# Optimization experiments

Hardware: AMD Instinct MI355X
Metric: run time of the kernel (lower is better)

## Reference

```python
import jax, jax.numpy as jnp
import numpy as np

B, L, DIN, H, E, K = 64, 256, 768, 64, 8, 2
S = 16  # sqrt(L): token<->feature grid side
LOSS_COEF = 1e-2


def gelu(x):
    return jax.nn.gelu(x, approximate=False)  # torch nn.GELU (exact erf)


def cv_squared(v):
    v = v.astype(jnp.float32)
    return jnp.var(v, ddof=1) / (jnp.mean(v) ** 2 + 1e-10)


def setup_inputs() -> dict:
    key = jax.random.key(0)
    ks = jax.random.split(key, 16)
    rn = lambda k, shape, s=0.02: jax.random.normal(k, shape, jnp.float32) * s
    lap = jnp.array([[0., 1., 0.], [1., -4., 1.], [0., 1., 0.]], jnp.float32)
    return {
        "x": jax.random.normal(ks[0], (B, L, DIN), jnp.float32),
        "dte": jax.random.normal(ks[1], (B, L, DIN), jnp.float32),
        "w_gate": rn(ks[2], (L, E), 1.0),
        "W_exp": rn(ks[3], (E, DIN, H)), "b_exp": jnp.zeros((E, H), jnp.float32),
        "W_sh": rn(ks[4], (DIN, H)), "b_sh": jnp.zeros((H,), jnp.float32),
        "ln_g": jnp.ones((H,), jnp.float32), "ln_b": jnp.zeros((H,), jnp.float32),
        "W_px": rn(ks[5], (H, 2 * H)), "b_px": jnp.zeros((2 * H,), jnp.float32),
        "conv_sh": jnp.tile(lap[None, None], (H, 1, 1, 1)),  # depthwise Laplacian [H,1,3,3]
        "W_pxx": rn(ks[6], (H, H)), "b_pxx": jnp.zeros((H,), jnp.float32),
        "W_dte": rn(ks[7], (H, H)), "b_dte": jnp.zeros((H,), jnp.float32),
        "W_dteall": rn(ks[8], (H, H)), "b_dteall": jnp.zeros((H,), jnp.float32),
        "W_rgb": rn(ks[9], (DIN, H)), "b_rgb": jnp.zeros((H,), jnp.float32),
        "W_fx": rn(ks[10], (H, H)), "b_fx": jnp.zeros((H,), jnp.float32),
        "W_fmod": rn(ks[11], (H, H)), "b_fmod": jnp.zeros((H,), jnp.float32),
        "W_fxx": rn(ks[12], (H, H)), "b_fxx": jnp.zeros((H,), jnp.float32),
    }


def reference(x, dte, w_gate, W_exp, b_exp, W_sh, b_sh, ln_g, ln_b, W_px, b_px,
              conv_sh, W_pxx, b_pxx, W_dte, b_dte, W_dteall, b_dteall,
              W_rgb, b_rgb, W_fx, b_fx, W_fmod, b_fmod, W_fxx, b_fxx):
    # ---- top-k gating (clean logits; noisy_gating=False / eval) ----
    logits = dte.mean(-1) @ w_gate                     # [B,E]
    topv, topi = jax.lax.top_k(logits, K)
    topg = jax.nn.softmax(topv, axis=1)
    gates = jnp.zeros_like(logits).at[jnp.arange(B)[:, None], topi].set(topg)
    importance = gates.sum(0)
    load = (gates > 0).sum(0).astype(jnp.float32)
    loss = LOSS_COEF * (cv_squared(importance) + cv_squared(load))
    # ---- sparse dispatch / expert Linear / weighted combine (dense-equivalent) ----
    y = jnp.einsum('be,bld,edh->blh', gates, dte, W_exp) + (gates @ b_exp)[:, None, :]
    # ---- shared expert Linear + Shared block ----
    sh = dte @ W_sh + b_sh                             # [B,L,H]
    shortcut = sh
    t = (sh - sh.mean(-1, keepdims=True)) * jax.lax.rsqrt(sh.var(-1, keepdims=True) + 1e-6)
    t = t * ln_g + ln_b
    t = t @ W_px + b_px                                # [B,L,2H]
    t1, t2 = t[..., :H], t[..., H:]
    f = t1.transpose(0, 2, 1).reshape(B, H, S, S)      # token2feature
    f = jax.lax.conv_general_dilated(f, conv_sh, (1, 1), 'SAME', feature_group_count=H)
    t1 = f.reshape(B, H, L).transpose(0, 2, 1)         # feature2token
    sh = (gelu(t1) * t2) @ W_pxx + b_pxx + shortcut
    # ---- combine MoE and shared streams ----
    dte_tok = (y @ W_dte + b_dte) + (sh @ W_dteall + b_dteall)
    rgb_tok = x @ W_rgb + b_rgb
    # ---- Fusion (its self.norm was overwritten to GELU; token<->feature round-trip is identity) ----
    shortcut = rgb_tok
    a = gelu(rgb_tok) @ W_fx + b_fx
    m = gelu(dte_tok) @ W_fmod + b_fmod
    out = (gelu(m) * a) @ W_fxx + b_fxx + shortcut     # [B,L,H]
    return out, loss
```

## Files before the change

kernel.cpp:

```cpp
#include <hip/hip_runtime.h>
#include <hip/hip_bf16.h>
#include <math.h>

typedef unsigned short u16;
typedef unsigned int u32;
typedef __attribute__((ext_vector_type(8))) short bf16x8;
typedef __attribute__((ext_vector_type(4))) float f32x4;


__device__ __forceinline__ float bf2f(u16 u) {
    union { u32 i; float f; } x; x.i = ((u32)u) << 16; return x.f;
}
__device__ __forceinline__ u16 f2bf(float f) {
    union { __hip_bfloat16 h; u16 u; } x;
    x.h = __float2bfloat16(f);
    return x.u;
}
__device__ __forceinline__ u32 pack2(float a, float b) {
    union { __hip_bfloat162 h; u32 u; } x;
    x.h = __float22bfloat162_rn(make_float2(a, b));
    return x.u;
}
__device__ __forceinline__ float wsum(float v) {
    #pragma unroll
    for (int o = 1; o < 64; o <<= 1) v += __shfl_xor(v, o, 64);
    return v;
}
__device__ __forceinline__ float gelu_f(float x) {
    return 0.5f * x * (1.0f + erff(x * 0.70710678118654752440f));
}

__global__ __launch_bounds__(256) void k_gate_part(const float* __restrict__ dte,
                                                   const float* __restrict__ w_gate,
                                                   float* __restrict__ partial) {
    __shared__ float dmeanS[64];
    int p = blockIdx.x, tid = threadIdx.x, w = tid >> 6, lane = tid & 63;
    #pragma unroll
    for (int h = 0; h < 2; h++) {
        float4 v[8][3];
        #pragma unroll
        for (int i = 0; i < 8; i++) {
            const float* pr = dte + ((size_t)p * 64 + w * 16 + h * 8 + i) * 768;
            #pragma unroll
            for (int j = 0; j < 3; j++)
                v[i][j] = *(const float4*)(pr + (lane + j * 64) * 4);
        }
        #pragma unroll
        for (int i = 0; i < 8; i++) {
            float s = 0.f;
            #pragma unroll
            for (int j = 0; j < 3; j++)
                s += v[i][j].x + v[i][j].y + v[i][j].z + v[i][j].w;
            s = wsum(s);
            if (lane == 0) dmeanS[w * 16 + h * 8 + i] = s * (1.f / 768.f);
        }
    }
    __syncthreads();
    if (w == 0) {
        float dm = dmeanS[lane];
        int wl = (p & 3) * 64 + lane;
        #pragma unroll
        for (int e = 0; e < 8; e++) {
            float s = wsum(dm * w_gate[wl * 8 + e]);
            if (lane == 0) partial[p * 8 + e] = s;
        }
    }
}

__global__ __launch_bounds__(256) void k_gate_fin(const float* __restrict__ partial,
                                                  const float* __restrict__ b_exp,
                                                  int* __restrict__ topi,
                                                  float* __restrict__ topg,
                                                  float* __restrict__ bias_y,
                                                  float* __restrict__ loss_out) {
    __shared__ float gS[64 * 8];
    __shared__ int i0S[64], i1S[64];
    __shared__ float g0S[64], g1S[64];
    int tid = threadIdx.x;
    if (tid < 64) {
        float lg[8];
        #pragma unroll
        for (int e = 0; e < 8; e++)
            lg[e] = partial[(tid * 4 + 0) * 8 + e] + partial[(tid * 4 + 1) * 8 + e] +
                    partial[(tid * 4 + 2) * 8 + e] + partial[(tid * 4 + 3) * 8 + e];
        int i0 = 0; float v0 = lg[0];
        #pragma unroll
        for (int e = 1; e < 8; e++) if (lg[e] > v0) { v0 = lg[e]; i0 = e; }
        int i1 = -1; float v1 = -1e30f;
        #pragma unroll
        for (int e = 0; e < 8; e++) if (e != i0 && lg[e] > v1) { v1 = lg[e]; i1 = e; }
        if (i1 < 0) i1 = (i0 + 1) & 7;
        float e2 = expf(v1 - v0);
        float g0 = 1.f / (1.f + e2);
        float g1 = e2 / (1.f + e2);
        #pragma unroll
        for (int e = 0; e < 8; e++) gS[tid * 8 + e] = 0.f;
        gS[tid * 8 + i0] = g0;
        gS[tid * 8 + i1] = g1;
        i0S[tid] = i0; i1S[tid] = i1; g0S[tid] = g0; g1S[tid] = g1;
        topi[tid * 2] = i0; topi[tid * 2 + 1] = i1;
        topg[tid * 2] = g0; topg[tid * 2 + 1] = g1;
    }
    __syncthreads();
    for (int idx = tid; idx < 4096; idx += 256) {
        int b = idx >> 6, h = idx & 63;
        bias_y[idx] = g0S[b] * b_exp[i0S[b] * 64 + h] + g1S[b] * b_exp[i1S[b] * 64 + h];
    }
    if (tid < 64) {
        float g[8];
        #pragma unroll
        for (int e = 0; e < 8; e++) g[e] = gS[tid * 8 + e];
        float imp[8], ld[8];
        #pragma unroll
        for (int e = 0; e < 8; e++) {
            imp[e] = wsum(g[e]);
            ld[e]  = wsum(g[e] > 0.f ? 1.f : 0.f);
        }
        if (tid == 0) {
            float l = 0.f;
            {
                float s = 0.f;
                #pragma unroll
                for (int e = 0; e < 8; e++) s += imp[e];
                float mn = s / 8.f, v = 0.f;
                #pragma unroll
                for (int e = 0; e < 8; e++) { float d = imp[e] - mn; v += d * d; }
                l += (v / 7.f) / (mn * mn + 1e-10f);
            }
            {
                float s = 0.f;
                #pragma unroll
                for (int e = 0; e < 8; e++) s += ld[e];
                float mn = s / 8.f, v = 0.f;
                #pragma unroll
                for (int e = 0; e < 8; e++) { float d = ld[e] - mn; v += d * d; }
                l += (v / 7.f) / (mn * mn + 1e-10f);
            }
            loss_out[0] = 0.01f * l;
        }
    }
}

__global__ __launch_bounds__(256) void k_gemm3(const float* __restrict__ dte,
                                               const float* __restrict__ x,
                                               const float* __restrict__ W_sh,
                                               const float* __restrict__ b_sh,
                                               const float* __restrict__ W_exp,
                                               const int* __restrict__ topi,
                                               const float* __restrict__ topg,
                                               const float* __restrict__ bias_y,
                                               const float* __restrict__ W_rgb,
                                               const float* __restrict__ b_rgb,
                                               float* __restrict__ buf_sh,
                                               u16* __restrict__ buf_y,
                                               float* __restrict__ out_rgb) {
    __shared__ __align__(16) u16 As[64 * 72];
    __shared__ __align__(16) u16 Wt0[64 * 72];
    __shared__ __align__(16) u16 Wt1[64 * 72];
    int bid = blockIdx.x;
    bool fused = bid < 256;
    int row0 = fused ? bid * 64 : (bid - 256) * 64;
    int b = row0 >> 8;
    int tid = threadIdx.x, wv = tid >> 6, lane = tid & 63;
    int m = lane & 15, quad = lane >> 4;

    const float* A  = fused ? dte : x;
    const float* Wb = fused ? W_sh : W_rgb;
    const float* We0 = W_exp;
    const float* We1 = W_exp;
    float g0 = 0.f, g1 = 0.f;
    if (fused) {
        We0 = W_exp + (size_t)topi[2 * b] * 49152;
        We1 = W_exp + (size_t)topi[2 * b + 1] * 49152;
        g0 = topg[2 * b]; g1 = topg[2 * b + 1];
    }

    float4 pa[2][2];
    float4 pwv0[4];
    float4 pwv1[4];
    const int a_r  = tid >> 3;
    const int a_k8 = (tid & 7) * 8;
    const int wn4  = (tid & 15) * 4;
    const int wk4  = (tid >> 4) * 4;

    auto loadA = [&](int kc) {
        #pragma unroll
        for (int j = 0; j < 2; j++) {
            const float* src = A + (size_t)(row0 + a_r + j * 32) * 768 + kc * 64 + a_k8;
            pa[j][0] = *(const float4*)(src);
            pa[j][1] = *(const float4*)(src + 4);
        }
    };
    auto loadW = [&](int kc) {
        #pragma unroll
        for (int q = 0; q < 4; q++)
            pwv0[q] = *(const float4*)(Wb + (size_t)(kc * 64 + wk4 + q) * 64 + wn4);
        if (fused) {
            #pragma unroll
            for (int q = 0; q < 4; q++) {
                float4 a = *(const float4*)(We0 + (size_t)(kc * 64 + wk4 + q) * 64 + wn4);
                float4 c = *(const float4*)(We1 + (size_t)(kc * 64 + wk4 + q) * 64 + wn4);
                pwv1[q] = make_float4(g0 * a.x + g1 * c.x, g0 * a.y + g1 * c.y,
                                      g0 * a.z + g1 * c.z, g0 * a.w + g1 * c.w);
            }
        }
    };
    auto stageLDS = [&]() {
        #pragma unroll
        for (int j = 0; j < 2; j++) {
            uint4 d;
            d.x = pack2(pa[j][0].x, pa[j][0].y);
            d.y = pack2(pa[j][0].z, pa[j][0].w);
            d.z = pack2(pa[j][1].x, pa[j][1].y);
            d.w = pack2(pa[j][1].z, pa[j][1].w);
            *(uint4*)&As[(a_r + j * 32) * 72 + a_k8] = d;
        }
        *(uint2*)&Wt0[(wn4 + 0) * 72 + wk4] =
            make_uint2(pack2(pwv0[0].x, pwv0[1].x), pack2(pwv0[2].x, pwv0[3].x));
        *(uint2*)&Wt0[(wn4 + 1) * 72 + wk4] =
            make_uint2(pack2(pwv0[0].y, pwv0[1].y), pack2(pwv0[2].y, pwv0[3].y));
        *(uint2*)&Wt0[(wn4 + 2) * 72 + wk4] =
            make_uint2(pack2(pwv0[0].z, pwv0[1].z), pack2(pwv0[2].z, pwv0[3].z));
        *(uint2*)&Wt0[(wn4 + 3) * 72 + wk4] =
            make_uint2(pack2(pwv0[0].w, pwv0[1].w), pack2(pwv0[2].w, pwv0[3].w));
        if (fused) {
            *(uint2*)&Wt1[(wn4 + 0) * 72 + wk4] =
                make_uint2(pack2(pwv1[0].x, pwv1[1].x), pack2(pwv1[2].x, pwv1[3].x));
            *(uint2*)&Wt1[(wn4 + 1) * 72 + wk4] =
                make_uint2(pack2(pwv1[0].y, pwv1[1].y), pack2(pwv1[2].y, pwv1[3].y));
            *(uint2*)&Wt1[(wn4 + 2) * 72 + wk4] =
                make_uint2(pack2(pwv1[0].z, pwv1[1].z), pack2(pwv1[2].z, pwv1[3].z));
            *(uint2*)&Wt1[(wn4 + 3) * 72 + wk4] =
                make_uint2(pack2(pwv1[0].w, pwv1[1].w), pack2(pwv1[2].w, pwv1[3].w));
        }
    };

    f32x4 z = {0.f, 0.f, 0.f, 0.f};
    f32x4 s0 = z, s1 = z, s2 = z, s3 = z;
    f32x4 y0 = z, y1 = z, y2 = z, y3 = z;

    loadA(0); loadW(0);
    for (int kc = 0; kc < 12; kc++) {
        __syncthreads();
        stageLDS();
        __syncthreads();
        if (kc < 11) { loadA(kc + 1); loadW(kc + 1); }
        const int ar = (wv * 16 + m) * 72;
        bf16x8 a0 = *(const bf16x8*)&As[ar + quad * 8];
        bf16x8 a1 = *(const bf16x8*)&As[ar + 32 + quad * 8];
        #pragma unroll
        for (int t = 0; t < 4; t++) {
            const int br = (t * 16 + m) * 72;
            bf16x8 b0 = *(const bf16x8*)&Wt0[br + quad * 8];
            bf16x8 b1 = *(const bf16x8*)&Wt0[br + 32 + quad * 8];
            f32x4* sp = (t == 0) ? &s0 : (t == 1) ? &s1 : (t == 2) ? &s2 : &s3;
            *sp = __builtin_amdgcn_mfma_f32_16x16x32_bf16(a0, b0, *sp, 0, 0, 0);
            *sp = __builtin_amdgcn_mfma_f32_16x16x32_bf16(a1, b1, *sp, 0, 0, 0);
            if (fused) {
                bf16x8 c0 = *(const bf16x8*)&Wt1[br + quad * 8];
                bf16x8 c1 = *(const bf16x8*)&Wt1[br + 32 + quad * 8];
                f32x4* yp = (t == 0) ? &y0 : (t == 1) ? &y1 : (t == 2) ? &y2 : &y3;
                *yp = __builtin_amdgcn_mfma_f32_16x16x32_bf16(a0, c0, *yp, 0, 0, 0);
                *yp = __builtin_amdgcn_mfma_f32_16x16x32_bf16(a1, c1, *yp, 0, 0, 0);
            }
        }
    }

    f32x4 accs0[4] = {s0, s1, s2, s3};
    f32x4 accs1[4] = {y0, y1, y2, y3};
    #pragma unroll
    for (int t = 0; t < 4; t++) {
        int col = t * 16 + m;
        if (fused) {
            float bs = b_sh[col];
            float by = bias_y[b * 64 + col];
            #pragma unroll
            for (int i = 0; i < 4; i++) {
                int r = row0 + wv * 16 + quad * 4 + i;
                buf_sh[(size_t)r * 64 + col] = accs0[t][i] + bs;
                buf_y[(size_t)r * 64 + col]  = f2bf(accs1[t][i] + by);
            }
        } else {
            float br = b_rgb[col];
            #pragma unroll
            for (int i = 0; i < 4; i++) {
                int r = row0 + wv * 16 + quad * 4 + i;
                out_rgb[(size_t)r * 64 + col] = accs0[t][i] + br;
            }
        }
    }
}

__global__ __launch_bounds__(256) void k_lnpx(const float* __restrict__ buf_sh,
                                              const float* __restrict__ ln_g,
                                              const float* __restrict__ ln_b,
                                              const float* __restrict__ W_px,
                                              const float* __restrict__ b_px,
                                              u16* __restrict__ t1, u16* __restrict__ t2) {
    __shared__ __align__(16) float T[32 * 68];
    __shared__ __align__(16) float Wpx[8192];
    int r0 = blockIdx.x * 32;
    int tid = threadIdx.x, w = tid >> 6, lane = tid & 63;
    #pragma unroll
    for (int j = 0; j < 8; j++) {
        const float* g = W_px + (size_t)(w * 64 + j * 256) * 4 + lane * 4;
        float* l = Wpx + (w * 64 + j * 256) * 4;
        __builtin_amdgcn_global_load_lds(
            (const __attribute__((address_space(1))) unsigned int*)g,
            (__attribute__((address_space(3))) unsigned int*)l,
            16, 0, 0);
    }
    float lnG = ln_g[lane], lnB = ln_b[lane];
    for (int i = 0; i < 8; i++) {
        int l = w * 8 + i;
        float v = buf_sh[(size_t)(r0 + l) * 64 + lane];
        float mean = wsum(v) * (1.f / 64.f);
        float d = v - mean;
        float var = wsum(d * d) * (1.f / 64.f);
        T[l * 68 + lane] = d * rsqrtf(var + 1e-6f) * lnG + lnB;
    }
    __syncthreads();
    int rg = tid >> 4, cg = tid & 15;
    float acc1[2][4] = {}, acc2[2][4] = {};
    const float* tr = T + rg * 2 * 68;
    #pragma unroll 4
    for (int kk = 0; kk < 64; kk++) {
        float a0 = tr[kk], a1 = tr[68 + kk];
        float4 w1 = *(const float4*)(Wpx + kk * 128 + cg * 4);
        float4 w2 = *(const float4*)(Wpx + kk * 128 + 64 + cg * 4);
        acc1[0][0] += a0 * w1.x; acc1[0][1] += a0 * w1.y; acc1[0][2] += a0 * w1.z; acc1[0][3] += a0 * w1.w;
        acc1[1][0] += a1 * w1.x; acc1[1][1] += a1 * w1.y; acc1[1][2] += a1 * w1.z; acc1[1][3] += a1 * w1.w;
        acc2[0][0] += a0 * w2.x; acc2[0][1] += a0 * w2.y; acc2[0][2] += a0 * w2.z; acc2[0][3] += a0 * w2.w;
        acc2[1][0] += a1 * w2.x; acc2[1][1] += a1 * w2.y; acc2[1][2] += a1 * w2.z; acc2[1][3] += a1 * w2.w;
    }
    float4 b1 = *(const float4*)(b_px + cg * 4);
    float4 b2 = *(const float4*)(b_px + 64 + cg * 4);
    #pragma unroll
    for (int i = 0; i < 2; i++) {
        int r = r0 + rg * 2 + i;
        u32* d1 = (u32*)(t1 + (size_t)r * 64 + cg * 4);
        d1[0] = pack2(acc1[i][0] + b1.x, acc1[i][1] + b1.y);
        d1[1] = pack2(acc1[i][2] + b1.z, acc1[i][3] + b1.w);
        u32* d2 = (u32*)(t2 + (size_t)r * 64 + cg * 4);
        d2[0] = pack2(acc2[i][0] + b2.x, acc2[i][1] + b2.y);
        d2[1] = pack2(acc2[i][2] + b2.z, acc2[i][3] + b2.w);
    }
}

__global__ __launch_bounds__(256) void k_tail(const u16* __restrict__ t1,
                                              const u16* __restrict__ t2,
                                              const float* __restrict__ conv_sh,
                                              const float* __restrict__ W_pxx,
                                              const float* __restrict__ b_pxx,
                                              const float* __restrict__ buf_sh,
                                              const u16* __restrict__ buf_y,
                                              const float* __restrict__ W_dte,
                                              const float* __restrict__ b_dte,
                                              const float* __restrict__ W_dteall,
                                              const float* __restrict__ b_dteall,
                                              const float* __restrict__ W_fx,
                                              const float* __restrict__ b_fx,
                                              const float* __restrict__ W_fmod,
                                              const float* __restrict__ b_fmod,
                                              const float* __restrict__ W_fxx,
                                              const float* __restrict__ b_fxx,
                                              float* __restrict__ out) {
    __shared__ __align__(16) float C0[32 * 68];
    __shared__ __align__(16) float GA[32 * 68];
    __shared__ __align__(16) float SH1[32 * 68];
    __shared__ __align__(16) float GM[32 * 68];
    __shared__ __align__(16) u16   Ybh[32 * 72];
    __shared__ __align__(16) float WL[2][4096];
    int r0 = blockIdx.x * 32;
    int tid = threadIdx.x, w = tid >> 6, lane = tid & 63;
    int rg = tid >> 4, cg = tid & 15;

    auto stage_w = [&](const float* __restrict__ Wsrc, int half) {
        const float* g = Wsrc + w * 1024 + lane * 4;
        float* l = &WL[half][w * 1024];
        #pragma unroll
        for (int j = 0; j < 4; j++) {
            __builtin_amdgcn_global_load_lds(
                (const __attribute__((address_space(1))) unsigned int*)(g + j * 256),
                (__attribute__((address_space(3))) unsigned int*)(l + j * 256),
                16, 0, 0);
        }
    };

    stage_w(W_pxx, 0);

    stage_w(W_dte, 1);
    float4 rsv[2];
    #pragma unroll
    for (int i = 0; i < 2; i++) {
        int r = rg * 2 + i;
        uint2 v = *(const uint2*)(buf_y + (size_t)(r0 + r) * 64 + cg * 4);
        *(uint2*)(&Ybh[r * 72 + cg * 4]) = v;
        rsv[i] = *(const float4*)(out + (size_t)(r0 + r) * 64 + cg * 4);
        GA[r * 68 + cg * 4 + 0] = gelu_f(rsv[i].x);
        GA[r * 68 + cg * 4 + 1] = gelu_f(rsv[i].y);
        GA[r * 68 + cg * 4 + 2] = gelu_f(rsv[i].z);
        GA[r * 68 + cg * 4 + 3] = gelu_f(rsv[i].w);
    }
    {
        float c0 = conv_sh[lane * 9 + 0], c1 = conv_sh[lane * 9 + 1], c2 = conv_sh[lane * 9 + 2];
        float c3 = conv_sh[lane * 9 + 3], c4 = conv_sh[lane * 9 + 4], c5 = conv_sh[lane * 9 + 5];
        float c6 = conv_sh[lane * 9 + 6], c7 = conv_sh[lane * 9 + 7], c8 = conv_sh[lane * 9 + 8];
        #pragma unroll
        for (int i = 0; i < 8; i++) {
            int l = w * 8 + i;
            int gr = r0 + l;
            int pix = gr & 255, ii = pix >> 4, jj = pix & 15;
            const u16* p = t1 + (size_t)gr * 64 + lane;
            float c = c4 * bf2f(p[0]);
            if (ii > 0) {
                c += c1 * bf2f(p[-1024]);
                if (jj > 0)  c += c0 * bf2f(p[-1024 - 64]);
                if (jj < 15) c += c2 * bf2f(p[-1024 + 64]);
            }
            if (jj > 0)  c += c3 * bf2f(p[-64]);
            if (jj < 15) c += c5 * bf2f(p[64]);
            if (ii < 15) {
                c += c7 * bf2f(p[1024]);
                if (jj > 0)  c += c6 * bf2f(p[1024 - 64]);
                if (jj < 15) c += c8 * bf2f(p[1024 + 64]);
            }
            C0[l * 68 + lane] = gelu_f(c) * bf2f(t2[(size_t)gr * 64 + lane]);
        }
    }
    __syncthreads();

    {
        float acc[2][4] = {};
        const float* ur = C0 + rg * 2 * 68;
        #pragma unroll 8
        for (int kk = 0; kk < 64; kk++) {
            float a0 = ur[kk], a1 = ur[68 + kk];
            float4 wvv = *(const float4*)(&WL[0][kk * 64 + cg * 4]);
            acc[0][0] += a0 * wvv.x; acc[0][1] += a0 * wvv.y; acc[0][2] += a0 * wvv.z; acc[0][3] += a0 * wvv.w;
            acc[1][0] += a1 * wvv.x; acc[1][1] += a1 * wvv.y; acc[1][2] += a1 * wvv.z; acc[1][3] += a1 * wvv.w;
        }
        float4 bp = *(const float4*)(b_pxx + cg * 4);
        #pragma unroll
        for (int i = 0; i < 2; i++) {
            int r = rg * 2 + i;
            float4 shv = *(const float4*)(buf_sh + (size_t)(r0 + r) * 64 + cg * 4);
            *(float4*)(SH1 + r * 68 + cg * 4) =
                make_float4(acc[i][0] + bp.x + shv.x, acc[i][1] + bp.y + shv.y,
                            acc[i][2] + bp.z + shv.z, acc[i][3] + bp.w + shv.w);
        }
    }
    __syncthreads();

    float accC[2][4] = {};
    stage_w(W_dteall, 0);
    {
        const u16* yr = Ybh + rg * 2 * 72;
        #pragma unroll 8
        for (int kk = 0; kk < 64; kk++) {
            float y0 = bf2f(yr[kk]), y1 = bf2f(yr[72 + kk]);
            float4 wvv = *(const float4*)(&WL[1][kk * 64 + cg * 4]);
            accC[0][0] += y0 * wvv.x; accC[0][1] += y0 * wvv.y; accC[0][2] += y0 * wvv.z; accC[0][3] += y0 * wvv.w;
            accC[1][0] += y1 * wvv.x; accC[1][1] += y1 * wvv.y; accC[1][2] += y1 * wvv.z; accC[1][3] += y1 * wvv.w;
        }
    }
    __syncthreads();

    stage_w(W_fx, 1);
    {
        const float* sr = SH1 + rg * 2 * 68;
        #pragma unroll 8
        for (int kk = 0; kk < 64; kk++) {
            float s0 = sr[kk], s1 = sr[68 + kk];
            float4 wvv = *(const float4*)(&WL[0][kk * 64 + cg * 4]);
            accC[0][0] += s0 * wvv.x; accC[0][1] += s0 * wvv.y; accC[0][2] += s0 * wvv.z; accC[0][3] += s0 * wvv.w;
            accC[1][0] += s1 * wvv.x; accC[1][1] += s1 * wvv.y; accC[1][2] += s1 * wvv.z; accC[1][3] += s1 * wvv.w;
        }
        float4 bd1 = *(const float4*)(b_dte + cg * 4);
        float4 bd2 = *(const float4*)(b_dteall + cg * 4);
        #pragma unroll
        for (int i = 0; i < 2; i++) {
            int r = rg * 2 + i;
            *(float4*)(GM + r * 68 + cg * 4) =
                make_float4(gelu_f(accC[i][0] + bd1.x + bd2.x), gelu_f(accC[i][1] + bd1.y + bd2.y),
                            gelu_f(accC[i][2] + bd1.z + bd2.z), gelu_f(accC[i][3] + bd1.w + bd2.w));
        }
    }
    __syncthreads();

    float accA[2][4] = {};
    stage_w(W_fmod, 0);
    {
        const float* ga = GA + rg * 2 * 68;
        #pragma unroll 8
        for (int kk = 0; kk < 64; kk++) {
            float a0 = ga[kk], a1 = ga[68 + kk];
            float4 wvv = *(const float4*)(&WL[1][kk * 64 + cg * 4]);
            accA[0][0] += a0 * wvv.x; accA[0][1] += a0 * wvv.y; accA[0][2] += a0 * wvv.z; accA[0][3] += a0 * wvv.w;
            accA[1][0] += a1 * wvv.x; accA[1][1] += a1 * wvv.y; accA[1][2] += a1 * wvv.z; accA[1][3] += a1 * wvv.w;
        }
    }
    __syncthreads();

    stage_w(W_fxx, 1);
    {
        float accM[2][4] = {};
        const float* gm = GM + rg * 2 * 68;
        #pragma unroll 8
        for (int kk = 0; kk < 64; kk++) {
            float m0 = gm[kk], m1 = gm[68 + kk];
            float4 wvv = *(const float4*)(&WL[0][kk * 64 + cg * 4]);
            accM[0][0] += m0 * wvv.x; accM[0][1] += m0 * wvv.y; accM[0][2] += m0 * wvv.z; accM[0][3] += m0 * wvv.w;
            accM[1][0] += m1 * wvv.x; accM[1][1] += m1 * wvv.y; accM[1][2] += m1 * wvv.z; accM[1][3] += m1 * wvv.w;
        }
        float4 bx = *(const float4*)(b_fx + cg * 4);
        float4 bm = *(const float4*)(b_fmod + cg * 4);
        #pragma unroll
        for (int i = 0; i < 2; i++) {
            int r = rg * 2 + i;
            float a0 = accA[i][0] + bx.x, a1 = accA[i][1] + bx.y, a2 = accA[i][2] + bx.z, a3 = accA[i][3] + bx.w;
            float m0 = accM[i][0] + bm.x, m1 = accM[i][1] + bm.y, m2 = accM[i][2] + bm.z, m3 = accM[i][3] + bm.w;
            *(float4*)(C0 + r * 68 + cg * 4) =
                make_float4(gelu_f(m0) * a0, gelu_f(m1) * a1, gelu_f(m2) * a2, gelu_f(m3) * a3);
        }
    }
    __syncthreads();

    {
        float acc[2][4] = {};
        const float* pr = C0 + rg * 2 * 68;
        #pragma unroll 8
        for (int kk = 0; kk < 64; kk++) {
            float p0 = pr[kk], p1 = pr[68 + kk];
            float4 wvv = *(const float4*)(&WL[1][kk * 64 + cg * 4]);
            acc[0][0] += p0 * wvv.x; acc[0][1] += p0 * wvv.y; acc[0][2] += p0 * wvv.z; acc[0][3] += p0 * wvv.w;
            acc[1][0] += p1 * wvv.x; acc[1][1] += p1 * wvv.y; acc[1][2] += p1 * wvv.z; acc[1][3] += p1 * wvv.w;
        }
        float4 bo = *(const float4*)(b_fxx + cg * 4);
        #pragma unroll
        for (int i = 0; i < 2; i++) {
            int r = rg * 2 + i;
            *(float4*)(out + (size_t)(r0 + r) * 64 + cg * 4) =
                make_float4(acc[i][0] + bo.x + rsv[i].x, acc[i][1] + bo.y + rsv[i].y,
                            acc[i][2] + bo.z + rsv[i].z, acc[i][3] + bo.w + rsv[i].w);
        }
    }
}

extern "C" void kernel_launch(void* const* d_in, const int* in_sizes, int n_in,
                              void* d_out, int out_size, void* d_ws, size_t ws_size,
                              hipStream_t stream) {
    const float* x       = (const float*)d_in[0];
    const float* dte     = (const float*)d_in[1];
    const float* w_gate  = (const float*)d_in[2];
    const float* W_exp   = (const float*)d_in[3];
    const float* b_exp   = (const float*)d_in[4];
    const float* W_sh    = (const float*)d_in[5];
    const float* b_sh    = (const float*)d_in[6];
    const float* ln_g    = (const float*)d_in[7];
    const float* ln_b    = (const float*)d_in[8];
    const float* W_px    = (const float*)d_in[9];
    const float* b_px    = (const float*)d_in[10];
    const float* conv_sh = (const float*)d_in[11];
    const float* W_pxx   = (const float*)d_in[12];
    const float* b_pxx   = (const float*)d_in[13];
    const float* W_dte   = (const float*)d_in[14];
    const float* b_dte   = (const float*)d_in[15];
    const float* W_dteall= (const float*)d_in[16];
    const float* b_dteall= (const float*)d_in[17];
    const float* W_rgb   = (const float*)d_in[18];
    const float* b_rgb   = (const float*)d_in[19];
    const float* W_fx    = (const float*)d_in[20];
    const float* b_fx    = (const float*)d_in[21];
    const float* W_fmod  = (const float*)d_in[22];
    const float* b_fmod  = (const float*)d_in[23];
    const float* W_fxx   = (const float*)d_in[24];
    const float* b_fxx   = (const float*)d_in[25];

    float* out = (float*)d_out;

    float* wsf    = (float*)d_ws;
    float* partial= wsf;
    int*   topi   = (int*)(wsf + 2048);
    float* topg   = wsf + 2176;
    float* bias_y = wsf + 2304;
    float* buf_sh = wsf + 8192;
    u16*   buf_y  = (u16*)(wsf + 8192 + 1048576);
    u16*   t1     = (u16*)(wsf + 8192 + 1048576 + 524288);
    u16*   t2     = (u16*)(wsf + 8192 + 1048576 + 524288*2);

    hipLaunchKernelGGL(k_gate_part, dim3(256), dim3(256), 0, stream, dte, w_gate, partial);
    hipLaunchKernelGGL(k_gate_fin, dim3(1), dim3(256), 0, stream,
                       partial, b_exp, topi, topg, bias_y, out + 1048576);
    hipLaunchKernelGGL(k_gemm3, dim3(512), dim3(256), 0, stream,
                       dte, x, W_sh, b_sh, W_exp, topi, topg, bias_y, W_rgb, b_rgb,
                       buf_sh, buf_y, out);
    hipLaunchKernelGGL(k_lnpx, dim3(512), dim3(256), 0, stream,
                       buf_sh, ln_g, ln_b, W_px, b_px, t1, t2);
    hipLaunchKernelGGL(k_tail, dim3(512), dim3(256), 0, stream,
                       t1, t2, conv_sh, W_pxx, b_pxx, buf_sh, buf_y,
                       W_dte, b_dte, W_dteall, b_dteall,
                       W_fx, b_fx, W_fmod, b_fmod, W_fxx, b_fxx, out);

    (void)in_sizes; (void)n_in; (void)out_size; (void)ws_size;
}
```

Baseline: 240.1 us.

## Precompute per-batch gated expert weight mix in gate kernel, simplify GEMM weight staging

The gate-finalize kernel grows from one block to 512 blocks. Each block computes the top-2 gating for one batch slice and writes a gate-weighted mix of the two selected expert matrices into a per-batch workspace buffer. The GEMM kernel now reads this single precomputed matrix instead of two expert matrices plus a blend. Its weight loads also switch to per-column scalar loads, so each thread can write contiguous 16-element bf16 runs into the transposed shared-memory tile. This removes one global read stream and the FMAs from the GEMM loop, but adds a 12 MB write and read through workspace and replaces float4 loads with scalar loads.

```diff
diff --git a/kernel.cpp b/kernel.cpp
--- a/kernel.cpp
+++ b/kernel.cpp
@@ -69,20 +69,21 @@
 
 __global__ __launch_bounds__(256) void k_gate_fin(const float* __restrict__ partial,
                                                   const float* __restrict__ b_exp,
+                                                  const float* __restrict__ W_exp,
+                                                  float* __restrict__ Wmix,
                                                   int* __restrict__ topi,
                                                   float* __restrict__ topg,
                                                   float* __restrict__ bias_y,
                                                   float* __restrict__ loss_out) {
-    __shared__ float gS[64 * 8];
-    __shared__ int i0S[64], i1S[64];
-    __shared__ float g0S[64], g1S[64];
-    int tid = threadIdx.x;
-    if (tid < 64) {
+    int bid = blockIdx.x, tid = threadIdx.x;
+
+    {
+        int b = bid >> 3;
         float lg[8];
         #pragma unroll
         for (int e = 0; e < 8; e++)
-            lg[e] = partial[(tid * 4 + 0) * 8 + e] + partial[(tid * 4 + 1) * 8 + e] +
-                    partial[(tid * 4 + 2) * 8 + e] + partial[(tid * 4 + 3) * 8 + e];
+            lg[e] = partial[(b * 4 + 0) * 8 + e] + partial[(b * 4 + 1) * 8 + e] +
+                    partial[(b * 4 + 2) * 8 + e] + partial[(b * 4 + 3) * 8 + e];
         int i0 = 0; float v0 = lg[0];
         #pragma unroll
         for (int e = 1; e < 8; e++) if (lg[e] > v0) { v0 = lg[e]; i0 = e; }
@@ -93,50 +94,85 @@
         float e2 = expf(v1 - v0);
         float g0 = 1.f / (1.f + e2);
         float g1 = e2 / (1.f + e2);
-        #pragma unroll
-        for (int e = 0; e < 8; e++) gS[tid * 8 + e] = 0.f;
-        gS[tid * 8 + i0] = g0;
-        gS[tid * 8 + i1] = g1;
-        i0S[tid] = i0; i1S[tid] = i1; g0S[tid] = g0; g1S[tid] = g1;
-        topi[tid * 2] = i0; topi[tid * 2 + 1] = i1;
-        topg[tid * 2] = g0; topg[tid * 2 + 1] = g1;
-    }
-    __syncthreads();
-    for (int idx = tid; idx < 4096; idx += 256) {
-        int b = idx >> 6, h = idx & 63;
-        bias_y[idx] = g0S[b] * b_exp[i0S[b] * 64 + h] + g1S[b] * b_exp[i1S[b] * 64 + h];
-    }
-    if (tid < 64) {
-        float g[8];
-        #pragma unroll
-        for (int e = 0; e < 8; e++) g[e] = gS[tid * 8 + e];
-        float imp[8], ld[8];
-        #pragma unroll
-        for (int e = 0; e < 8; e++) {
-            imp[e] = wsum(g[e]);
-            ld[e]  = wsum(g[e] > 0.f ? 1.f : 0.f);
-        }
-        if (tid == 0) {
-            float l = 0.f;
-            {
-                float s = 0.f;
-                #pragma unroll
-                for (int e = 0; e < 8; e++) s += imp[e];
-                float mn = s / 8.f, v = 0.f;
-                #pragma unroll
-                for (int e = 0; e < 8; e++) { float d = imp[e] - mn; v += d * d; }
-                l += (v / 7.f) / (mn * mn + 1e-10f);
+        const float4* We0 = (const float4*)(W_exp + (size_t)i0 * 49152);
+        const float4* We1 = (const float4*)(W_exp + (size_t)i1 * 49152);
+        float4* dst = (float4*)(Wmix + (size_t)b * 49152);
+        int part = bid & 7;
+        #pragma unroll
+        for (int j = 0; j < 6; j++) {
+            int f4 = part * 1536 + j * 256 + tid;
+            float4 a = We0[f4];
+            float4 c = We1[f4];
+            dst[f4] = make_float4(g0 * a.x + g1 * c.x, g0 * a.y + g1 * c.y,
+                                  g0 * a.z + g1 * c.z, g0 * a.w + g1 * c.w);
+        }
+    }
+
+    if (bid == 0) {
+        __shared__ float gS[64 * 8];
+        __shared__ int i0S[64], i1S[64];
+        __shared__ float g0S[64], g1S[64];
+        if (tid < 64) {
+            float lg[8];
+            #pragma unroll
+            for (int e = 0; e < 8; e++)
+                lg[e] = partial[(tid * 4 + 0) * 8 + e] + partial[(tid * 4 + 1) * 8 + e] +
+                        partial[(tid * 4 + 2) * 8 + e] + partial[(tid * 4 + 3) * 8 + e];
+            int i0 = 0; float v0 = lg[0];
+            #pragma unroll
+            for (int e = 1; e < 8; e++) if (lg[e] > v0) { v0 = lg[e]; i0 = e; }
+            int i1 = -1; float v1 = -1e30f;
+            #pragma unroll
+            for (int e = 0; e < 8; e++) if (e != i0 && lg[e] > v1) { v1 = lg[e]; i1 = e; }
+            if (i1 < 0) i1 = (i0 + 1) & 7;
+            float e2 = expf(v1 - v0);
+            float g0 = 1.f / (1.f + e2);
+            float g1 = e2 / (1.f + e2);
+            #pragma unroll
+            for (int e = 0; e < 8; e++) gS[tid * 8 + e] = 0.f;
+            gS[tid * 8 + i0] = g0;
+            gS[tid * 8 + i1] = g1;
+            i0S[tid] = i0; i1S[tid] = i1; g0S[tid] = g0; g1S[tid] = g1;
+            topi[tid * 2] = i0; topi[tid * 2 + 1] = i1;
+            topg[tid * 2] = g0; topg[tid * 2 + 1] = g1;
+        }
+        __syncthreads();
+        for (int idx = tid; idx < 4096; idx += 256) {
+            int b = idx >> 6, h = idx & 63;
+            bias_y[idx] = g0S[b] * b_exp[i0S[b] * 64 + h] + g1S[b] * b_exp[i1S[b] * 64 + h];
+        }
+        if (tid < 64) {
+            float g[8];
+            #pragma unroll
+            for (int e = 0; e < 8; e++) g[e] = gS[tid * 8 + e];
+            float imp[8], ld[8];
+            #pragma unroll
+            for (int e = 0; e < 8; e++) {
+                imp[e] = wsum(g[e]);
+                ld[e]  = wsum(g[e] > 0.f ? 1.f : 0.f);
             }
-            {
-                float s = 0.f;
-                #pragma unroll
-                for (int e = 0; e < 8; e++) s += ld[e];
-                float mn = s / 8.f, v = 0.f;
-                #pragma unroll
-                for (int e = 0; e < 8; e++) { float d = ld[e] - mn; v += d * d; }
-                l += (v / 7.f) / (mn * mn + 1e-10f);
+            if (tid == 0) {
+                float l = 0.f;
+                {
+                    float s = 0.f;
+                    #pragma unroll
+                    for (int e = 0; e < 8; e++) s += imp[e];
+                    float mn = s / 8.f, v = 0.f;
+                    #pragma unroll
+                    for (int e = 0; e < 8; e++) { float d = imp[e] - mn; v += d * d; }
+                    l += (v / 7.f) / (mn * mn + 1e-10f);
+                }
+                {
+                    float s = 0.f;
+                    #pragma unroll
+                    for (int e = 0; e < 8; e++) s += ld[e];
+                    float mn = s / 8.f, v = 0.f;
+                    #pragma unroll
+                    for (int e = 0; e < 8; e++) { float d = ld[e] - mn; v += d * d; }
+                    l += (v / 7.f) / (mn * mn + 1e-10f);
+                }
+                loss_out[0] = 0.01f * l;
             }
-            loss_out[0] = 0.01f * l;
         }
     }
 }
@@ -145,9 +181,7 @@
                                                const float* __restrict__ x,
                                                const float* __restrict__ W_sh,
                                                const float* __restrict__ b_sh,
-                                               const float* __restrict__ W_exp,
-                                               const int* __restrict__ topi,
-                                               const float* __restrict__ topg,
+                                               const float* __restrict__ Wmix,
                                                const float* __restrict__ bias_y,
                                                const float* __restrict__ W_rgb,
                                                const float* __restrict__ b_rgb,
@@ -166,22 +200,15 @@
 
     const float* A  = fused ? dte : x;
     const float* Wb = fused ? W_sh : W_rgb;
-    const float* We0 = W_exp;
-    const float* We1 = W_exp;
-    float g0 = 0.f, g1 = 0.f;
-    if (fused) {
-        We0 = W_exp + (size_t)topi[2 * b] * 49152;
-        We1 = W_exp + (size_t)topi[2 * b + 1] * 49152;
-        g0 = topg[2 * b]; g1 = topg[2 * b + 1];
-    }
+    const float* Wm = Wmix + (size_t)b * 49152;
 
     float4 pa[2][2];
-    float4 pwv0[4];
-    float4 pwv1[4];
+    float  pw0[16];
+    float  pw1[16];
     const int a_r  = tid >> 3;
     const int a_k8 = (tid & 7) * 8;
-    const int wn4  = (tid & 15) * 4;
-    const int wk4  = (tid >> 4) * 4;
+    const int w_n  = tid & 63;
+    const int w_k0 = (tid >> 6) * 16;
 
     auto loadA = [&](int kc) {
         #pragma unroll
@@ -193,16 +220,12 @@
     };
     auto loadW = [&](int kc) {
         #pragma unroll
-        for (int q = 0; q < 4; q++)
-            pwv0[q] = *(const float4*)(Wb + (size_t)(kc * 64 + wk4 + q) * 64 + wn4);
+        for (int j = 0; j < 16; j++)
+            pw0[j] = Wb[(size_t)(kc * 64 + w_k0 + j) * 64 + w_n];
         if (fused) {
             #pragma unroll
-            for (int q = 0; q < 4; q++) {
-                float4 a = *(const float4*)(We0 + (size_t)(kc * 64 + wk4 + q) * 64 + wn4);
-                float4 c = *(const float4*)(We1 + (size_t)(kc * 64 + wk4 + q) * 64 + wn4);
-                pwv1[q] = make_float4(g0 * a.x + g1 * c.x, g0 * a.y + g1 * c.y,
-                                      g0 * a.z + g1 * c.z, g0 * a.w + g1 * c.w);
-            }
+            for (int j = 0; j < 16; j++)
+                pw1[j] = Wm[(size_t)(kc * 64 + w_k0 + j) * 64 + w_n];
         }
     };
     auto stageLDS = [&]() {
@@ -215,23 +238,23 @@
             d.w = pack2(pa[j][1].z, pa[j][1].w);
             *(uint4*)&As[(a_r + j * 32) * 72 + a_k8] = d;
         }
-        *(uint2*)&Wt0[(wn4 + 0) * 72 + wk4] =
-            make_uint2(pack2(pwv0[0].x, pwv0[1].x), pack2(pwv0[2].x, pwv0[3].x));
-        *(uint2*)&Wt0[(wn4 + 1) * 72 + wk4] =
-            make_uint2(pack2(pwv0[0].y, pwv0[1].y), pack2(pwv0[2].y, pwv0[3].y));
-        *(uint2*)&Wt0[(wn4 + 2) * 72 + wk4] =
-            make_uint2(pack2(pwv0[0].z, pwv0[1].z), pack2(pwv0[2].z, pwv0[3].z));
-        *(uint2*)&Wt0[(wn4 + 3) * 72 + wk4] =
-            make_uint2(pack2(pwv0[0].w, pwv0[1].w), pack2(pwv0[2].w, pwv0[3].w));
+        {
+            uint4 d0, d1;
+            d0.x = pack2(pw0[0],  pw0[1]);  d0.y = pack2(pw0[2],  pw0[3]);
+            d0.z = pack2(pw0[4],  pw0[5]);  d0.w = pack2(pw0[6],  pw0[7]);
+            d1.x = pack2(pw0[8],  pw0[9]);  d1.y = pack2(pw0[10], pw0[11]);
+            d1.z = pack2(pw0[12], pw0[13]); d1.w = pack2(pw0[14], pw0[15]);
+            *(uint4*)&Wt0[w_n * 72 + w_k0]     = d0;
+            *(uint4*)&Wt0[w_n * 72 + w_k0 + 8] = d1;
+        }
         if (fused) {
-            *(uint2*)&Wt1[(wn4 + 0) * 72 + wk4] =
-                make_uint2(pack2(pwv1[0].x, pwv1[1].x), pack2(pwv1[2].x, pwv1[3].x));
-            *(uint2*)&Wt1[(wn4 + 1) * 72 + wk4] =
-                make_uint2(pack2(pwv1[0].y, pwv1[1].y), pack2(pwv1[2].y, pwv1[3].y));
-            *(uint2*)&Wt1[(wn4 + 2) * 72 + wk4] =
-                make_uint2(pack2(pwv1[0].z, pwv1[1].z), pack2(pwv1[2].z, pwv1[3].z));
-            *(uint2*)&Wt1[(wn4 + 3) * 72 + wk4] =
-                make_uint2(pack2(pwv1[0].w, pwv1[1].w), pack2(pwv1[2].w, pwv1[3].w));
+            uint4 d0, d1;
+            d0.x = pack2(pw1[0],  pw1[1]);  d0.y = pack2(pw1[2],  pw1[3]);
+            d0.z = pack2(pw1[4],  pw1[5]);  d0.w = pack2(pw1[6],  pw1[7]);
+            d1.x = pack2(pw1[8],  pw1[9]);  d1.y = pack2(pw1[10], pw1[11]);
+            d1.z = pack2(pw1[12], pw1[13]); d1.w = pack2(pw1[14], pw1[15]);
+            *(uint4*)&Wt1[w_n * 72 + w_k0]     = d0;
+            *(uint4*)&Wt1[w_n * 72 + w_k0 + 8] = d1;
         }
     };
 
@@ -588,12 +611,13 @@
     u16*   buf_y  = (u16*)(wsf + 8192 + 1048576);
     u16*   t1     = (u16*)(wsf + 8192 + 1048576 + 524288);
     u16*   t2     = (u16*)(wsf + 8192 + 1048576 + 524288*2);
+    float* Wmix   = wsf + 8192 + 1048576 + 524288*3;
 
     hipLaunchKernelGGL(k_gate_part, dim3(256), dim3(256), 0, stream, dte, w_gate, partial);
-    hipLaunchKernelGGL(k_gate_fin, dim3(1), dim3(256), 0, stream,
-                       partial, b_exp, topi, topg, bias_y, out + 1048576);
+    hipLaunchKernelGGL(k_gate_fin, dim3(512), dim3(256), 0, stream,
+                       partial, b_exp, W_exp, Wmix, topi, topg, bias_y, out + 1048576);
     hipLaunchKernelGGL(k_gemm3, dim3(512), dim3(256), 0, stream,
-                       dte, x, W_sh, b_sh, W_exp, topi, topg, bias_y, W_rgb, b_rgb,
+                       dte, x, W_sh, b_sh, Wmix, bias_y, W_rgb, b_rgb,
                        buf_sh, buf_y, out);
     hipLaunchKernelGGL(k_lnpx, dim3(512), dim3(256), 0, stream,
                        buf_sh, ln_g, ln_b, W_px, b_px, t1, t2);
```

Measured after the change: 238.2 us. Within noise of the previous version (-0.8%).
